# Performance work log

Measured on AMD Instinct MI355X. Metric: run time of the kernel, lower is better.

Reference implementation:

```python
import jax, jax.numpy as jnp
import numpy as np

H = 8        # num_heads
DH = 64      # head_dim
DV = 64      # value_dim
DQ = 256     # query_dim
DHIT = 256   # hit_feature_dim
DMLP = 512   # query_dim * mlp_hidden_dim_multiplier
EPS = 1e-5


def _layernorm(x, g, b):
    m = jnp.mean(x, axis=-1, keepdims=True)
    v = jnp.mean(jnp.square(x - m), axis=-1, keepdims=True)
    return (x - m) * jax.lax.rsqrt(v + EPS) * g + b


def setup_inputs() -> dict:
    key = jax.random.key(0)
    ks = jax.random.split(key, 10)
    B, K, N = 8, 64, 16384
    s = 0.02
    return {
        "slot_representations": jax.random.normal(ks[0], (B, K, DQ), jnp.float32),
        "hit_features": jax.random.normal(ks[1], (B, N, DHIT), jnp.float32),
        "ln1_g": jnp.ones((DQ,), jnp.float32),
        "ln1_b": jnp.zeros((DQ,), jnp.float32),
        "Wq": jax.random.normal(ks[2], (DQ, H * DH), jnp.float32) * s,
        "Wk": jax.random.normal(ks[3], (DHIT, H * DH), jnp.float32) * s,
        "Wv": jax.random.normal(ks[4], (DHIT, H * DV), jnp.float32) * s,
        "W1": jax.random.normal(ks[5], (H * DV, DMLP), jnp.float32) * s,
        "b1": jnp.zeros((DMLP,), jnp.float32),
        "W2": jax.random.normal(ks[6], (DMLP, DQ), jnp.float32) * s,
        "b2": jnp.zeros((DQ,), jnp.float32),
        "ln2_g": jnp.ones((DQ,), jnp.float32),
        "ln2_b": jnp.zeros((DQ,), jnp.float32),
    }


def reference(slot_representations, hit_features, ln1_g, ln1_b, Wq, Wk, Wv,
              W1, b1, W2, b2, ln2_g, ln2_b):
    B, K, _ = slot_representations.shape
    _, N, _ = hit_features.shape
    scale = DH ** -0.5
    slots_norm = _layernorm(slot_representations, ln1_g, ln1_b)
    q = (slots_norm @ Wq).reshape(B, K, H, DH)          # [B,K,H,DH]
    k = (hit_features @ Wk).reshape(B, N, H, DH)        # [B,N,H,DH]
    v = (hit_features @ Wv).reshape(B, N, H, DV)        # [B,N,H,DV]
    logits = jnp.einsum('bkhd,bnhd->bhkn', q, k) * scale
    attn = jax.nn.softmax(logits, axis=-1)              # [B,H,K,N]
    att_v = jnp.einsum('bhkn,bnhd->bkhd', attn, v).reshape(B, K, H * DV)
    mlp_out = jax.nn.relu(att_v @ W1 + b1) @ W2 + b2
    return _layernorm(slot_representations + mlp_out, ln2_g, ln2_b)
```

## Files before the change

kernel.cpp:

```cpp
#include <hip/hip_runtime.h>
#include <hip/hip_bf16.h>

#define HH   8
#define Bb   8
#define Kk   64
#define Nn   16384
#define DQd  256
#define EPSf 1e-5f
#define NCH  32
#define CHK  512
#define SUB  32
#define NSUB (CHK / SUB)

typedef __bf16 bf16_t;
typedef __bf16 bf16x8 __attribute__((ext_vector_type(8)));
typedef __bf16 bf16x4 __attribute__((ext_vector_type(4)));
typedef __bf16 bf16x2 __attribute__((ext_vector_type(2)));
typedef float  f32x4  __attribute__((ext_vector_type(4)));
typedef float  f32x16 __attribute__((ext_vector_type(16)));

#define MFMA16(a, b, c) __builtin_amdgcn_mfma_f32_16x16x32_bf16((a), (b), (c), 0, 0, 0)
#define MFMA32(a, b, c) __builtin_amdgcn_mfma_f32_32x32x16_bf16((a), (b), (c), 0, 0, 0)

static __device__ __forceinline__ int pk2(float x, float y) {
    bf16x2 v; v[0] = (bf16_t)x; v[1] = (bf16_t)y;
    return __builtin_bit_cast(int, v);
}

static __device__ __forceinline__ void pack_tile(const f32x16 Sv, int hi, bf16x8* out) {
    #pragma unroll
    for (int kc = 0; kc < 2; ++kc) {
        const int oc = kc * 8;
        int Lp0 = pk2(Sv[oc + 0], Sv[oc + 1]);
        int Lp1 = pk2(Sv[oc + 2], Sv[oc + 3]);
        int Hp0 = pk2(Sv[oc + 4], Sv[oc + 5]);
        int Hp1 = pk2(Sv[oc + 6], Sv[oc + 7]);
        int Lx0 = __shfl_xor(Lp0, 32, 64);
        int Lx1 = __shfl_xor(Lp1, 32, 64);
        int Hx0 = __shfl_xor(Hp0, 32, 64);
        int Hx1 = __shfl_xor(Hp1, 32, 64);
        int4 bi;
        bi.x = hi ? Hx0 : Lp0;
        bi.y = hi ? Hx1 : Lp1;
        bi.z = hi ? Hp0 : Lx0;
        bi.w = hi ? Hp1 : Lx1;
        out[kc] = __builtin_bit_cast(bf16x8, bi);
    }
}

static __device__ __forceinline__ void store8(bf16_t* dst, float4 a, float4 b) {
    bf16x8 o;
    o[0] = (bf16_t)a.x; o[1] = (bf16_t)a.y; o[2] = (bf16_t)a.z; o[3] = (bf16_t)a.w;
    o[4] = (bf16_t)b.x; o[5] = (bf16_t)b.y; o[6] = (bf16_t)b.z; o[7] = (bf16_t)b.w;
    *(bf16x8*)dst = o;
}

__global__ __launch_bounds__(256) void k1_qt(
    const float* __restrict__ slots, const float* __restrict__ g1,
    const float* __restrict__ bb1, const float* __restrict__ Wq,
    const float* __restrict__ Wk, const float* __restrict__ Wv,
    bf16_t* __restrict__ qt, bf16_t* __restrict__ WvT)
{
    __shared__ alignas(16) bf16_t nrow[64][264];
    __shared__ alignas(16) bf16_t wqT[64][264];
    __shared__ alignas(16) bf16_t qb[64][72];
    __shared__ alignas(16) bf16_t wkT[256][72];

    if (blockIdx.x >= 64) {
        const int h = blockIdx.x - 64;
        const int t = threadIdx.x;
        const int dv = t & 63, dq = t >> 6;
        #pragma unroll
        for (int i = 0; i < 16; ++i) {
            int d = dq * 64 + i * 4;
            bf16x4 o;
            #pragma unroll
            for (int j = 0; j < 4; ++j)
                o[j] = (bf16_t)Wv[(size_t)(d + j) * 512 + h * 64 + dv];
            *(bf16x4*)&WvT[(size_t)(h * 64 + dv) * 256 + d] = o;
        }
        return;
    }

    const int b = blockIdx.x >> 3, h = blockIdx.x & 7;
    const int t = threadIdx.x;
    const int w = t >> 6, lane = t & 63;
    const int l15 = lane & 15, quad = lane >> 4;

    {
        float4 gv = *(const float4*)&g1[lane * 4];
        float4 bv = *(const float4*)&bb1[lane * 4];
        #pragma unroll 2
        for (int i = 0; i < 16; ++i) {
            int row = w * 16 + i;
            float4 x = *(const float4*)&slots[((size_t)b * Kk + row) * DQd + lane * 4];
            float s = x.x + x.y + x.z + x.w;
            for (int m = 1; m < 64; m <<= 1) s += __shfl_xor(s, m, 64);
            float mean = s * (1.0f / 256.0f);
            float dx = x.x - mean, dy = x.y - mean, dz = x.z - mean, dw = x.w - mean;
            float v2 = dx * dx + dy * dy + dz * dz + dw * dw;
            for (int m = 1; m < 64; m <<= 1) v2 += __shfl_xor(v2, m, 64);
            float rs = rsqrtf(v2 * (1.0f / 256.0f) + EPSf);
            bf16x4 o;
            o[0] = (bf16_t)(dx * rs * gv.x + bv.x);
            o[1] = (bf16_t)(dy * rs * gv.y + bv.y);
            o[2] = (bf16_t)(dz * rs * gv.z + bv.z);
            o[3] = (bf16_t)(dw * rs * gv.w + bv.w);
            *(bf16x4*)&nrow[row][lane * 4] = o;
        }
    }
    {
        int d = t & 63, r4 = t >> 6;
        #pragma unroll 8
        for (int p = 0; p < 64; ++p) {
            int i = r4 + p * 4;
            wqT[d][i] = (bf16_t)Wq[(size_t)i * 512 + h * 64 + d];
            wkT[i][d] = (bf16_t)Wk[(size_t)i * 512 + h * 64 + d];
        }
    }
    __syncthreads();

    f32x4 acc1[4] = {};
    for (int ks = 0; ks < 8; ++ks) {
        bf16x8 a = *(const bf16x8*)&nrow[w * 16 + l15][ks * 32 + quad * 8];
        #pragma unroll
        for (int tt = 0; tt < 4; ++tt) {
            bf16x8 bfr = *(const bf16x8*)&wqT[tt * 16 + l15][ks * 32 + quad * 8];
            acc1[tt] = MFMA16(a, bfr, acc1[tt]);
        }
    }
    #pragma unroll
    for (int tt = 0; tt < 4; ++tt)
        #pragma unroll
        for (int r = 0; r < 4; ++r)
            qb[w * 16 + quad * 4 + r][tt * 16 + l15] = (bf16_t)(acc1[tt][r] * 0.125f);
    __syncthreads();

    f32x4 acc2[16] = {};
    for (int ks = 0; ks < 2; ++ks) {
        bf16x8 a = *(const bf16x8*)&qb[w * 16 + l15][ks * 32 + quad * 8];
        #pragma unroll
        for (int tt = 0; tt < 16; ++tt) {
            bf16x8 bfr = *(const bf16x8*)&wkT[tt * 16 + l15][ks * 32 + quad * 8];
            acc2[tt] = MFMA16(a, bfr, acc2[tt]);
        }
    }
    size_t base = (size_t)(b * HH + h) * 64;
    #pragma unroll
    for (int tt = 0; tt < 16; ++tt)
        #pragma unroll
        for (int r = 0; r < 4; ++r)
            qt[(base + w * 16 + quad * 4 + r) * 256 + tt * 16 + l15] = (bf16_t)acc2[tt][r];
}

__global__ __launch_bounds__(512) void k3_attn(
    const float* __restrict__ hit, const bf16_t* __restrict__ qt,
    const bf16_t* __restrict__ WvT, bf16_t* __restrict__ nump,
    float* __restrict__ lp)
{
    __shared__ alignas(16) bf16_t hs[2][SUB * 256];
    __shared__ alignas(16) bf16_t vb[2][16 * 512];

    const int bid = blockIdx.x;
    const int c  = bid & 31;
    const int hg = (bid >> 5) & 1;
    const int b  = bid >> 6;
    const int t  = threadIdx.x;
    const int w = t >> 6, lane = t & 63;
    const int l31 = lane & 31, hi = lane >> 5;
    const int hl = w >> 1;
    const int qh = w & 1;
    const int h  = hg * 4 + hl;
    const int bh = b * HH + h;

    bf16x8 qf[16], wf[16];
    {
        const bf16_t* qrow = qt + ((size_t)bh * 64 + qh * 32 + l31) * 256 + hi * 8;
        const bf16_t* wrow = WvT + ((size_t)(h * 64 + qh * 32 + l31)) * 256 + hi * 8;
        #pragma unroll
        for (int ks = 0; ks < 16; ++ks) {
            qf[ks] = *(const bf16x8*)(qrow + ks * 16);
            wf[ks] = *(const bf16x8*)(wrow + ks * 16);
        }
    }

    f32x16 accO = {};
    f32x16 accX = {};
    float ls = 0.f;

    const float* hbase = hit + ((size_t)b * Nn + c * CHK) * 256;
    const int row0 = t >> 5, g0 = t & 31;
    const int sw0 = (g0 ^ (row0 & 7)) * 8;
    const int sw1 = (g0 ^ ((row0 + 16) & 7)) * 8;

    float4 pA0, pA1, pB0, pB1;
#define PREFETCH(ss) do { \
        const float* s0_ = hbase + (size_t)(ss) * SUB * 256 + (size_t)row0 * 256 + g0 * 8; \
        pA0 = ((const float4*)s0_)[0]; pA1 = ((const float4*)s0_)[1]; \
        const float* s1_ = s0_ + 16 * 256; \
        pB0 = ((const float4*)s1_)[0]; pB1 = ((const float4*)s1_)[1]; \
    } while (0)

    PREFETCH(0);
    store8(&hs[0][row0 * 256 + sw0], pA0, pA1);
    store8(&hs[0][(row0 + 16) * 256 + sw1], pB0, pB1);
    PREFETCH(1);
    __syncthreads();

    const int xr = l31 & 7;

    for (int s = 0; s < NSUB; ++s) {
        const int cur = s & 1;
        const bf16_t* hrow = &hs[cur][l31 * 256];

        f32x16 St = {}, Vt = {};
        #pragma unroll
        for (int ks = 0; ks < 16; ++ks) {
            bf16x8 A = *(const bf16x8*)(hrow + (((2 * ks + hi) ^ xr) * 8));
            Vt = MFMA32(A, wf[ks], Vt);
            St = MFMA32(A, qf[ks], St);
        }

        if (s + 1 < NSUB) {
            store8(&hs[cur ^ 1][row0 * 256 + sw0], pA0, pA1);
            store8(&hs[cur ^ 1][(row0 + 16) * 256 + sw1], pB0, pB1);
        }
        if (s + 2 < NSUB) PREFETCH(s + 2);

        #pragma unroll
        for (int r = 0; r < 16; ++r) {
            float e = __expf(St[r]);
            St[r] = e;
            ls += e;
        }
        bf16x8 Pf[2];
        pack_tile(St, hi, Pf);
        {
            bf16x8 Vf[2];
            pack_tile(Vt, hi, Vf);
            *(bf16x8*)&vb[cur][((hl * 2 + 0) * 2 + qh) * 512 + lane * 8] = Vf[0];
            *(bf16x8*)&vb[cur][((hl * 2 + 1) * 2 + qh) * 512 + lane * 8] = Vf[1];
        }
        __syncthreads();

        {
            bf16x8 vo0 = *(const bf16x8*)&vb[cur][((hl * 2 + 0) * 2 + qh) * 512 + lane * 8];
            bf16x8 vx0 = *(const bf16x8*)&vb[cur][((hl * 2 + 0) * 2 + (1 - qh)) * 512 + lane * 8];
            bf16x8 vo1 = *(const bf16x8*)&vb[cur][((hl * 2 + 1) * 2 + qh) * 512 + lane * 8];
            bf16x8 vx1 = *(const bf16x8*)&vb[cur][((hl * 2 + 1) * 2 + (1 - qh)) * 512 + lane * 8];
            accO = MFMA32(Pf[0], vo0, accO);
            accX = MFMA32(Pf[0], vx0, accX);
            accO = MFMA32(Pf[1], vo1, accO);
            accX = MFMA32(Pf[1], vx1, accX);
        }
    }
#undef PREFETCH

    {
        float lt = ls + __shfl_xor(ls, 32, 64);
        if (hi == 0)
            lp[((size_t)bh * NCH + c) * 64 + qh * 32 + l31] = lt;
    }
    {
        size_t nbase = ((size_t)bh * NCH + c) * 64 * 64;
        #pragma unroll
        for (int r = 0; r < 16; ++r) {
            int q = qh * 32 + (r & 3) + 8 * (r >> 2) + 4 * hi;
            size_t ro = nbase + (size_t)q * 64;
            nump[ro + qh * 32 + l31]       = (bf16_t)accO[r];
            nump[ro + (1 - qh) * 32 + l31] = (bf16_t)accX[r];
        }
    }
}

__global__ __launch_bounds__(256) void k35_comb(
    const bf16_t* __restrict__ nump, const float* __restrict__ lp,
    bf16_t* __restrict__ X)
{
    const int bh = blockIdx.x >> 1, qhb = blockIdx.x & 1;
    const int b = bh >> 3, h = bh & 7;
    const int t = threadIdx.x;
    const int q = qhb * 32 + (t >> 3), g = t & 7;
    float s8[8] = {};
    float lsum = 0.f;
    #pragma unroll 4
    for (int cc = 0; cc < NCH; ++cc) {
        size_t base = ((size_t)bh * NCH + cc) * 64 + q;
        bf16x8 v = *(const bf16x8*)&nump[base * 64 + g * 8];
        #pragma unroll
        for (int j = 0; j < 8; ++j) s8[j] += (float)v[j];
        lsum += lp[base];
    }
    float inv = 1.0f / lsum;
    bf16x8 o;
    #pragma unroll
    for (int j = 0; j < 8; ++j) o[j] = (bf16_t)(s8[j] * inv);
    *(bf16x8*)&X[((size_t)b * 64 + q) * 512 + h * 64 + g * 8] = o;
}

__global__ __launch_bounds__(256) void k4a_mlp1(
    const bf16_t* __restrict__ X, const float* __restrict__ W1,
    const float* __restrict__ b1, bf16_t* __restrict__ H)
{
    __shared__ float scr[32 * 33];
    const int rt = blockIdx.x >> 4, ct = blockIdx.x & 15;
    const int t = threadIdx.x;
    const int w = t >> 6, lane = t & 63, l31 = lane & 31, hi = lane >> 5;
    const int colbase = ct * 32;

    for (int i = t; i < 32 * 33; i += 256) scr[i] = 0.f;

    const bf16_t* xrow = X + ((size_t)(rt * 32 + l31)) * 512 + hi * 8;
    f32x16 acc = {};
    #pragma unroll
    for (int k8 = 0; k8 < 8; ++k8) {
        int kc = w * 8 + k8;
        bf16x8 af;
        #pragma unroll
        for (int j = 0; j < 8; ++j)
            af[j] = (bf16_t)W1[(size_t)(kc * 16 + hi * 8 + j) * 512 + colbase + l31];
        bf16x8 bfr = *(const bf16x8*)(xrow + kc * 16);
        acc = MFMA32(af, bfr, acc);
    }
    __syncthreads();
    #pragma unroll
    for (int r = 0; r < 16; ++r) {
        int m = (r & 3) + 8 * (r >> 2) + 4 * hi;
        atomicAdd(&scr[m * 33 + l31], acc[r]);
    }
    __syncthreads();
    const float bia = b1[colbase + l31];
    #pragma unroll
    for (int jj = 0; jj < 4; ++jj) {
        int j = w * 4 + jj;
        float v = scr[l31 * 33 + hi * 16 + j] + bia;
        v = fmaxf(v, 0.f);
        H[((size_t)(rt * 32 + hi * 16 + j)) * 512 + colbase + l31] = (bf16_t)v;
    }
}

__global__ __launch_bounds__(256) void k4b_gemm(
    const bf16_t* __restrict__ H, const float* __restrict__ W2,
    const float* __restrict__ b2, const float* __restrict__ slots,
    float* __restrict__ ys)
{
    __shared__ float scr[32 * 33];
    const int b = blockIdx.x >> 4, rtt = (blockIdx.x >> 3) & 1, ct = blockIdx.x & 7;
    const int t = threadIdx.x;
    const int w = t >> 6, lane = t & 63, l31 = lane & 31, hi = lane >> 5;
    const int colbase = ct * 32;
    const int rowbase = b * 64 + rtt * 32;

    for (int i = t; i < 32 * 33; i += 256) scr[i] = 0.f;

    const bf16_t* hrow = H + ((size_t)(rowbase + l31)) * 512 + hi * 8;
    f32x16 acc = {};
    #pragma unroll
    for (int k8 = 0; k8 < 8; ++k8) {
        int kc = w * 8 + k8;
        bf16x8 af;
        #pragma unroll
        for (int j = 0; j < 8; ++j)
            af[j] = (bf16_t)W2[(size_t)(kc * 16 + hi * 8 + j) * 256 + colbase + l31];
        bf16x8 bfr = *(const bf16x8*)(hrow + kc * 16);
        acc = MFMA32(af, bfr, acc);
    }
    __syncthreads();
    #pragma unroll
    for (int r = 0; r < 16; ++r) {
        int m = (r & 3) + 8 * (r >> 2) + 4 * hi;
        atomicAdd(&scr[m * 33 + l31], acc[r]);
    }
    __syncthreads();
    const float b2c = b2[colbase + l31];
    #pragma unroll
    for (int jj = 0; jj < 4; ++jj) {
        int j = w * 4 + jj;
        int row = rowbase + hi * 16 + j;
        float v = scr[l31 * 33 + hi * 16 + j] + b2c
                + slots[(size_t)row * 256 + colbase + l31];
        ys[(size_t)row * 256 + colbase + l31] = v;
    }
}

__global__ __launch_bounds__(256) void k4c_ln2(
    const float* __restrict__ ys, const float* __restrict__ g2,
    const float* __restrict__ bb2, float* __restrict__ out)
{
    const int t = threadIdx.x;
    const int w = t >> 6, lane = t & 63;
    float4 gv = *(const float4*)&g2[lane * 4];
    float4 bv = *(const float4*)&bb2[lane * 4];
    #pragma unroll
    for (int rr = 0; rr < 2; ++rr) {
        int row = blockIdx.x * 8 + w * 2 + rr;
        float4 x = *(const float4*)&ys[(size_t)row * 256 + lane * 4];
        float s = x.x + x.y + x.z + x.w;
        for (int m = 1; m < 64; m <<= 1) s += __shfl_xor(s, m, 64);
        float mean = s * (1.0f / 256.0f);
        float dx = x.x - mean, dy = x.y - mean, dz = x.z - mean, dw = x.w - mean;
        float v2 = dx * dx + dy * dy + dz * dz + dw * dw;
        for (int m = 1; m < 64; m <<= 1) v2 += __shfl_xor(v2, m, 64);
        float rs = rsqrtf(v2 * (1.0f / 256.0f) + EPSf);
        float4 o;
        o.x = dx * rs * gv.x + bv.x;
        o.y = dy * rs * gv.y + bv.y;
        o.z = dz * rs * gv.z + bv.z;
        o.w = dw * rs * gv.w + bv.w;
        *(float4*)&out[(size_t)row * 256 + lane * 4] = o;
    }
}

extern "C" void kernel_launch(void* const* d_in, const int* in_sizes, int n_in,
                              void* d_out, int out_size, void* d_ws, size_t ws_size,
                              hipStream_t stream) {
    (void)in_sizes; (void)n_in; (void)out_size; (void)ws_size;
    const float* slots = (const float*)d_in[0];
    const float* hit   = (const float*)d_in[1];
    const float* g1    = (const float*)d_in[2];
    const float* bb1   = (const float*)d_in[3];
    const float* Wq    = (const float*)d_in[4];
    const float* Wk    = (const float*)d_in[5];
    const float* Wv    = (const float*)d_in[6];
    const float* W1    = (const float*)d_in[7];
    const float* b1v   = (const float*)d_in[8];
    const float* W2    = (const float*)d_in[9];
    const float* b2v   = (const float*)d_in[10];
    const float* g2    = (const float*)d_in[11];
    const float* bb2   = (const float*)d_in[12];
    float* out = (float*)d_out;

    char* wsp = (char*)d_ws;
    bf16_t* qt   = (bf16_t*)wsp;
    float*  ys   = (float*) wsp;
    bf16_t* WvT  = (bf16_t*)(wsp + (size_t)2097152);
    bf16_t* nump = (bf16_t*)(wsp + (size_t)2359296);
    float*  lp   = (float*) (wsp + (size_t)19136512);
    bf16_t* X    = (bf16_t*)(wsp + (size_t)19660800);
    bf16_t* H    = (bf16_t*)(wsp + (size_t)20185088);

    hipLaunchKernelGGL(k1_qt, dim3(72), dim3(256), 0, stream,
                       slots, g1, bb1, Wq, Wk, Wv, qt, WvT);
    hipLaunchKernelGGL(k3_attn, dim3(Bb * 2 * NCH), dim3(512), 0, stream,
                       hit, qt, WvT, nump, lp);
    hipLaunchKernelGGL(k35_comb, dim3(128), dim3(256), 0, stream,
                       nump, lp, X);
    hipLaunchKernelGGL(k4a_mlp1, dim3(256), dim3(256), 0, stream,
                       X, W1, b1v, H);
    hipLaunchKernelGGL(k4b_gemm, dim3(128), dim3(256), 0, stream,
                       H, W2, b2v, slots, ys);
    hipLaunchKernelGGL(k4c_ln2, dim3(64), dim3(256), 0, stream,
                       ys, g2, bb2, out);
}
```

Baseline: 291.9 us.

## Split query-prep into LayerNorm, Wq·Wkᵀ precompute, and norm×M GEMM kernels

Replaces the single 72-block query-prep kernel with three kernels. The first computes LayerNorm and transposes Wv. The second forms the per-head combined matrix Wq_h·Wk_hᵀ (scaled), and the third multiplies normalized slots by it to produce the query-key projection. This spreads the work over more blocks, uses 32x32 MFMA, and avoids each block reloading and transposing full Wq/Wk slices through scalar strided loads. It adds two kernel launches and an extra intermediate round trip through workspace memory, and it changes the bf16 rounding points.

After: 295.5 us. No clear change (+1.2%).

```diff
diff --git a/kernel.cpp b/kernel.cpp
--- a/kernel.cpp
+++ b/kernel.cpp
@@ -55,20 +55,14 @@
     *(bf16x8*)dst = o;
 }
 
-__global__ __launch_bounds__(256) void k1_qt(
+__global__ __launch_bounds__(256) void k0_ln(
     const float* __restrict__ slots, const float* __restrict__ g1,
-    const float* __restrict__ bb1, const float* __restrict__ Wq,
-    const float* __restrict__ Wk, const float* __restrict__ Wv,
-    bf16_t* __restrict__ qt, bf16_t* __restrict__ WvT)
-{
-    __shared__ alignas(16) bf16_t nrow[64][264];
-    __shared__ alignas(16) bf16_t wqT[64][264];
-    __shared__ alignas(16) bf16_t qb[64][72];
-    __shared__ alignas(16) bf16_t wkT[256][72];
-
-    if (blockIdx.x >= 64) {
-        const int h = blockIdx.x - 64;
-        const int t = threadIdx.x;
+    const float* __restrict__ bb1, const float* __restrict__ Wv,
+    bf16_t* __restrict__ norm, bf16_t* __restrict__ WvT)
+{
+    const int t = threadIdx.x;
+    if (blockIdx.x >= 32) {
+        const int h = blockIdx.x - 32;
         const int dv = t & 63, dq = t >> 6;
         #pragma unroll
         for (int i = 0; i < 16; ++i) {
@@ -81,76 +75,121 @@
         }
         return;
     }
-
-    const int b = blockIdx.x >> 3, h = blockIdx.x & 7;
-    const int t = threadIdx.x;
+    const int b = blockIdx.x >> 2, rg = blockIdx.x & 3;
     const int w = t >> 6, lane = t & 63;
-    const int l15 = lane & 15, quad = lane >> 4;
-
-    {
-        float4 gv = *(const float4*)&g1[lane * 4];
-        float4 bv = *(const float4*)&bb1[lane * 4];
-        #pragma unroll 2
-        for (int i = 0; i < 16; ++i) {
-            int row = w * 16 + i;
-            float4 x = *(const float4*)&slots[((size_t)b * Kk + row) * DQd + lane * 4];
-            float s = x.x + x.y + x.z + x.w;
-            for (int m = 1; m < 64; m <<= 1) s += __shfl_xor(s, m, 64);
-            float mean = s * (1.0f / 256.0f);
-            float dx = x.x - mean, dy = x.y - mean, dz = x.z - mean, dw = x.w - mean;
-            float v2 = dx * dx + dy * dy + dz * dz + dw * dw;
-            for (int m = 1; m < 64; m <<= 1) v2 += __shfl_xor(v2, m, 64);
-            float rs = rsqrtf(v2 * (1.0f / 256.0f) + EPSf);
-            bf16x4 o;
-            o[0] = (bf16_t)(dx * rs * gv.x + bv.x);
-            o[1] = (bf16_t)(dy * rs * gv.y + bv.y);
-            o[2] = (bf16_t)(dz * rs * gv.z + bv.z);
-            o[3] = (bf16_t)(dw * rs * gv.w + bv.w);
-            *(bf16x4*)&nrow[row][lane * 4] = o;
-        }
-    }
-    {
-        int d = t & 63, r4 = t >> 6;
-        #pragma unroll 8
-        for (int p = 0; p < 64; ++p) {
-            int i = r4 + p * 4;
-            wqT[d][i] = (bf16_t)Wq[(size_t)i * 512 + h * 64 + d];
-            wkT[i][d] = (bf16_t)Wk[(size_t)i * 512 + h * 64 + d];
-        }
-    }
-    __syncthreads();
-
-    f32x4 acc1[4] = {};
-    for (int ks = 0; ks < 8; ++ks) {
-        bf16x8 a = *(const bf16x8*)&nrow[w * 16 + l15][ks * 32 + quad * 8];
-        #pragma unroll
-        for (int tt = 0; tt < 4; ++tt) {
-            bf16x8 bfr = *(const bf16x8*)&wqT[tt * 16 + l15][ks * 32 + quad * 8];
-            acc1[tt] = MFMA16(a, bfr, acc1[tt]);
-        }
-    }
-    #pragma unroll
-    for (int tt = 0; tt < 4; ++tt)
-        #pragma unroll
-        for (int r = 0; r < 4; ++r)
-            qb[w * 16 + quad * 4 + r][tt * 16 + l15] = (bf16_t)(acc1[tt][r] * 0.125f);
-    __syncthreads();
-
-    f32x4 acc2[16] = {};
-    for (int ks = 0; ks < 2; ++ks) {
-        bf16x8 a = *(const bf16x8*)&qb[w * 16 + l15][ks * 32 + quad * 8];
-        #pragma unroll
-        for (int tt = 0; tt < 16; ++tt) {
-            bf16x8 bfr = *(const bf16x8*)&wkT[tt * 16 + l15][ks * 32 + quad * 8];
-            acc2[tt] = MFMA16(a, bfr, acc2[tt]);
-        }
-    }
-    size_t base = (size_t)(b * HH + h) * 64;
-    #pragma unroll
-    for (int tt = 0; tt < 16; ++tt)
-        #pragma unroll
-        for (int r = 0; r < 4; ++r)
-            qt[(base + w * 16 + quad * 4 + r) * 256 + tt * 16 + l15] = (bf16_t)acc2[tt][r];
+    float4 gv = *(const float4*)&g1[lane * 4];
+    float4 bv = *(const float4*)&bb1[lane * 4];
+    #pragma unroll
+    for (int i = 0; i < 4; ++i) {
+        int row = rg * 16 + w * 4 + i;
+        float4 x = *(const float4*)&slots[((size_t)b * Kk + row) * DQd + lane * 4];
+        float s = x.x + x.y + x.z + x.w;
+        for (int m = 1; m < 64; m <<= 1) s += __shfl_xor(s, m, 64);
+        float mean = s * (1.0f / 256.0f);
+        float dx = x.x - mean, dy = x.y - mean, dz = x.z - mean, dw = x.w - mean;
+        float v2 = dx * dx + dy * dy + dz * dz + dw * dw;
+        for (int m = 1; m < 64; m <<= 1) v2 += __shfl_xor(v2, m, 64);
+        float rs = rsqrtf(v2 * (1.0f / 256.0f) + EPSf);
+        bf16x4 o;
+        o[0] = (bf16_t)(dx * rs * gv.x + bv.x);
+        o[1] = (bf16_t)(dy * rs * gv.y + bv.y);
+        o[2] = (bf16_t)(dz * rs * gv.z + bv.z);
+        o[3] = (bf16_t)(dw * rs * gv.w + bv.w);
+        *(bf16x4*)&norm[((size_t)b * Kk + row) * 256 + lane * 4] = o;
+    }
+}
+
+__global__ __launch_bounds__(256) void k0m(
+    const float* __restrict__ Wq, const float* __restrict__ Wk,
+    bf16_t* __restrict__ MT)
+{
+    __shared__ float scr4[4][32 * 33];
+    const int h = blockIdx.x >> 2, rt = blockIdx.x & 3;
+    const int t = threadIdx.x;
+    const int w = t >> 6, lane = t & 63, l31 = lane & 31, hi = lane >> 5;
+
+    f32x16 acc[2][2] = {};
+    for (int kc = 0; kc < 4; ++kc) {
+        bf16x8 af[2], bfr[2];
+        #pragma unroll
+        for (int mt = 0; mt < 2; ++mt) {
+            const float* src = &Wq[(size_t)(w * 64 + mt * 32 + l31) * 512 + h * 64 + kc * 16 + hi * 8];
+            float4 u0 = ((const float4*)src)[0], u1 = ((const float4*)src)[1];
+            af[mt][0] = (bf16_t)u0.x; af[mt][1] = (bf16_t)u0.y;
+            af[mt][2] = (bf16_t)u0.z; af[mt][3] = (bf16_t)u0.w;
+            af[mt][4] = (bf16_t)u1.x; af[mt][5] = (bf16_t)u1.y;
+            af[mt][6] = (bf16_t)u1.z; af[mt][7] = (bf16_t)u1.w;
+        }
+        #pragma unroll
+        for (int nt = 0; nt < 2; ++nt) {
+            const float* src = &Wk[(size_t)(rt * 64 + nt * 32 + l31) * 512 + h * 64 + kc * 16 + hi * 8];
+            float4 u0 = ((const float4*)src)[0], u1 = ((const float4*)src)[1];
+            bfr[nt][0] = (bf16_t)u0.x; bfr[nt][1] = (bf16_t)u0.y;
+            bfr[nt][2] = (bf16_t)u0.z; bfr[nt][3] = (bf16_t)u0.w;
+            bfr[nt][4] = (bf16_t)u1.x; bfr[nt][5] = (bf16_t)u1.y;
+            bfr[nt][6] = (bf16_t)u1.z; bfr[nt][7] = (bf16_t)u1.w;
+        }
+        #pragma unroll
+        for (int mt = 0; mt < 2; ++mt)
+            #pragma unroll
+            for (int nt = 0; nt < 2; ++nt)
+                acc[mt][nt] = MFMA32(af[mt], bfr[nt], acc[mt][nt]);
+    }
+    float* scr = scr4[w];
+    #pragma unroll
+    for (int mt = 0; mt < 2; ++mt)
+        for (int nt = 0; nt < 2; ++nt) {
+            #pragma unroll
+            for (int r = 0; r < 16; ++r) {
+                int m = (r & 3) + 8 * (r >> 2) + 4 * hi;
+                scr[m * 33 + l31] = acc[mt][nt][r] * 0.125f;
+            }
+            #pragma unroll
+            for (int j = 0; j < 16; ++j) {
+                int c = rt * 64 + nt * 32 + hi * 16 + j;
+                MT[((size_t)(h * 256 + c)) * 256 + w * 64 + mt * 32 + l31]
+                    = (bf16_t)scr[l31 * 33 + hi * 16 + j];
+            }
+        }
+}
+
+__global__ __launch_bounds__(256) void k1n(
+    const bf16_t* __restrict__ norm, const bf16_t* __restrict__ MT,
+    bf16_t* __restrict__ qt)
+{
+    __shared__ float scr4[4][32 * 33];
+    const int bid = blockIdx.x;
+    const int ch = bid & 1, h = (bid >> 1) & 7, b = bid >> 4;
+    const int t = threadIdx.x;
+    const int w = t >> 6, lane = t & 63, l31 = lane & 31, hi = lane >> 5;
+    const int colbase = ch * 128 + w * 32;
+
+    const bf16_t* mbase = MT + ((size_t)(h * 256 + colbase + l31)) * 256 + hi * 8;
+    const bf16_t* nbase = norm + ((size_t)(b * 64 + l31)) * 256 + hi * 8;
+
+    f32x16 acc[2] = {};
+    for (int kc = 0; kc < 16; ++kc) {
+        bf16x8 af = *(const bf16x8*)(mbase + kc * 16);
+        bf16x8 b0 = *(const bf16x8*)(nbase + kc * 16);
+        bf16x8 b1 = *(const bf16x8*)(nbase + (size_t)32 * 256 + kc * 16);
+        acc[0] = MFMA32(af, b0, acc[0]);
+        acc[1] = MFMA32(af, b1, acc[1]);
+    }
+    float* scr = scr4[w];
+    size_t qbase = (size_t)(b * HH + h) * 64;
+    #pragma unroll
+    for (int nt = 0; nt < 2; ++nt) {
+        #pragma unroll
+        for (int r = 0; r < 16; ++r) {
+            int m = (r & 3) + 8 * (r >> 2) + 4 * hi;
+            scr[m * 33 + l31] = acc[nt][r];
+        }
+        #pragma unroll
+        for (int j = 0; j < 16; ++j) {
+            qt[(qbase + nt * 32 + hi * 16 + j) * 256 + colbase + l31]
+                = (bf16_t)scr[l31 * 33 + hi * 16 + j];
+        }
+    }
 }
 
 __global__ __launch_bounds__(512) void k3_attn(
@@ -435,12 +474,18 @@
     float*  ys   = (float*) wsp;
     bf16_t* WvT  = (bf16_t*)(wsp + (size_t)2097152);
     bf16_t* nump = (bf16_t*)(wsp + (size_t)2359296);
+    bf16_t* MT   = (bf16_t*)(wsp + (size_t)2359296);
+    bf16_t* norm = (bf16_t*)(wsp + (size_t)2359296 + 1048576);
     float*  lp   = (float*) (wsp + (size_t)19136512);
     bf16_t* X    = (bf16_t*)(wsp + (size_t)19660800);
     bf16_t* H    = (bf16_t*)(wsp + (size_t)20185088);
 
-    hipLaunchKernelGGL(k1_qt, dim3(72), dim3(256), 0, stream,
-                       slots, g1, bb1, Wq, Wk, Wv, qt, WvT);
+    hipLaunchKernelGGL(k0_ln, dim3(40), dim3(256), 0, stream,
+                       slots, g1, bb1, Wv, norm, WvT);
+    hipLaunchKernelGGL(k0m, dim3(32), dim3(256), 0, stream,
+                       Wq, Wk, MT);
+    hipLaunchKernelGGL(k1n, dim3(128), dim3(256), 0, stream,
+                       norm, MT, qt);
     hipLaunchKernelGGL(k3_attn, dim3(Bb * 2 * NCH), dim3(512), 0, stream,
                        hit, qt, WvT, nump, lp);
     hipLaunchKernelGGL(k35_comb, dim3(128), dim3(256), 0, stream,
```
